# Performance work log

Measured on AMD Instinct MI355X. Metric: run time of the kernel, lower is better.

Reference implementation:

```python
import jax, jax.numpy as jnp
import numpy as np

EPS = float(np.finfo(np.float32).tiny)  # matches torch EPSILON
TAU = 0.1
K = 64  # self.k


def setup_inputs() -> dict:
    key = jax.random.key(0)
    k1, k2 = jax.random.split(key)
    bsz, Nmax, ensemble, train_ensemble = 64, 128, 2, 2
    scores = jax.random.normal(k1, (bsz, Nmax, Nmax, ensemble), dtype=jnp.float32)
    # Gumbel(0,1) noise, pre-sampled for determinism: g = -log(-log(U))
    u = jax.random.uniform(k2, (train_ensemble * bsz * ensemble, Nmax * Nmax),
                           dtype=jnp.float32, minval=1e-7, maxval=1.0 - 1e-7)
    gumbel = -jnp.log(-jnp.log(u))
    return {"scores": scores, "gumbel": gumbel, "train_ensemble": train_ensemble}


def reference(scores, gumbel, train_ensemble):
    # policy == 'global_topk_directed'
    bsz, Nmax, _, ensemble = scores.shape
    local_k = min(K, Nmax * Nmax)
    # (bsz, Nmax, Nmax, E) -> (bsz*E, Nmax^2)
    flat = scores.transpose(0, 3, 1, 2).reshape(bsz * ensemble, Nmax * Nmax)
    flat = jnp.tile(flat, (train_ensemble, 1)) + gumbel

    zeros = jnp.zeros_like(flat)

    def step(carry, _):
        f, khot, onehot = carry
        f = f + jnp.log(jnp.maximum(1.0 - onehot, EPS))
        onehot = jax.nn.softmax(f / TAU, axis=1)
        return (f, khot + onehot, onehot), None

    (flat, khot, _), _ = jax.lax.scan(step, (flat, zeros, zeros), None, length=local_k)

    # hard: straight-through k-hot via top-k scatter
    _, ind = jax.lax.top_k(khot, local_k)  # (R, local_k)
    rows = jnp.arange(khot.shape[0])[:, None]
    khot_hard = jnp.zeros_like(khot).at[rows, ind].set(1.0)
    res = khot_hard - jax.lax.stop_gradient(khot) + khot

    new_mask = res.reshape(train_ensemble, bsz, ensemble, Nmax, Nmax).transpose(0, 1, 3, 4, 2)
    return new_mask
```

## Files before the change

kernel.cpp:

```cpp
#include <hip/hip_runtime.h>
#include <math.h>


#define NWAVES  16
#define M_ELEMS 16384
#define EPT     16
#define KSEL    64
#define NCAND   256
#define CPL     4
#define NBINS   4096
#define THRESH  (M_ELEMS - NCAND)
#define C10     14.42695019f

template <int CTRL, int RM = 0xF>
__device__ __forceinline__ float dpp_f(float x, float identity) {
    return __int_as_float(__builtin_amdgcn_update_dpp(
        __float_as_int(identity), __float_as_int(x), CTRL, RM, 0xF, false));
}
template <int CTRL, int RM = 0xF>
__device__ __forceinline__ unsigned dpp_u(unsigned x, unsigned identity) {
    return (unsigned)__builtin_amdgcn_update_dpp(
        (int)identity, (int)x, CTRL, RM, 0xF, false);
}
__device__ __forceinline__ float wave_sum_bcast(float x) {
    x += dpp_f<0x111>(x, 0.0f);
    x += dpp_f<0x112>(x, 0.0f);
    x += dpp_f<0x114>(x, 0.0f);
    x += dpp_f<0x118>(x, 0.0f);
    x += dpp_f<0x142>(x, 0.0f);
    x += dpp_f<0x143>(x, 0.0f);
    return __int_as_float(__builtin_amdgcn_readlane(__float_as_int(x), 63));
}
__device__ __forceinline__ float wave_fmax_bcast(float x) {
    x = fmaxf(x, dpp_f<0x111>(x, -INFINITY));
    x = fmaxf(x, dpp_f<0x112>(x, -INFINITY));
    x = fmaxf(x, dpp_f<0x114>(x, -INFINITY));
    x = fmaxf(x, dpp_f<0x118>(x, -INFINITY));
    x = fmaxf(x, dpp_f<0x142>(x, -INFINITY));
    x = fmaxf(x, dpp_f<0x143>(x, -INFINITY));
    return __int_as_float(__builtin_amdgcn_readlane(__float_as_int(x), 63));
}
__device__ __forceinline__ unsigned wave_prefix_incl(unsigned x) {
    x += dpp_u<0x111>(x, 0u);
    x += dpp_u<0x112>(x, 0u);
    x += dpp_u<0x114>(x, 0u);
    x += dpp_u<0x118>(x, 0u);
    x += dpp_u<0x142, 0xA>(x, 0u);
    x += dpp_u<0x143, 0xC>(x, 0u);
    return x;
}

__global__ __launch_bounds__(1024, 4) void screen_kernel(
    const float* __restrict__ scores,
    const float* __restrict__ gumbel,
    float* __restrict__ cand_f,
    unsigned* __restrict__ cand_i,
    float* __restrict__ out)
{
    const int tid  = threadIdx.x;
    const int lane = tid & 63;
    const int wid  = tid >> 6;
    const int bid = blockIdx.x;
    const int r   = ((bid & 127) << 1) | (bid >> 7);
    const int t_ = r >> 7;
    const int be = r & 127;
    const int b  = be >> 1;
    const int e  = be & 1;

    __shared__ unsigned int hist[NBINS];
    __shared__ unsigned int wofs[NWAVES];
    __shared__ unsigned int cutbin;
    __shared__ unsigned int candcnt;

    float* orow = out + (size_t)(t_ * 64 + b) * (M_ELEMS * 2) + e;

    float fv[EPT];
    {
        const float* gum = gumbel + (size_t)r * M_ELEMS;
        const float* scb = scores + (size_t)b * (M_ELEMS * 2);
        #pragma unroll
        for (int g = 0; g < 4; ++g) {
            const int mb = (tid << 2) + (g << 12);
            const float4 gv = *reinterpret_cast<const float4*>(&gum[mb]);
            const float4 sa = *reinterpret_cast<const float4*>(&scb[(size_t)mb * 2]);
            const float4 sb = *reinterpret_cast<const float4*>(&scb[(size_t)mb * 2 + 4]);
            float s0, s1, s2, s3;
            if (e == 0) { s0 = sa.x; s1 = sa.z; s2 = sb.x; s3 = sb.z; }
            else        { s0 = sa.y; s1 = sa.w; s2 = sb.y; s3 = sb.w; }
            fv[g * 4 + 0] = s0 + gv.x;
            fv[g * 4 + 1] = s1 + gv.y;
            fv[g * 4 + 2] = s2 + gv.z;
            fv[g * 4 + 3] = s3 + gv.w;
        }
    }
    #pragma unroll
    for (int k = 0; k < NBINS / 1024; ++k) hist[tid + k * 1024] = 0u;
    __syncthreads();

    #pragma unroll
    for (int k = 0; k < EPT; ++k) {
        const unsigned u  = __float_as_uint(fv[k]);
        const unsigned tk = u ^ (unsigned)(((int)u >> 31) | 0x80000000);
        atomicAdd(&hist[tk >> 20], 1u);
    }
    __syncthreads();

    if (wid == 0) {
        unsigned part = 0;
        #pragma unroll 8
        for (int j = 0; j < 64; ++j)
            part += hist[(lane << 6) + ((j + lane) & 63)];
        const unsigned P = wave_prefix_incl(part);
        const unsigned long long mk = __ballot(P >= THRESH);
        const int L = __builtin_ctzll(mk);
        const unsigned base = (L > 0)
            ? (unsigned)__builtin_amdgcn_readlane((int)P, L - 1) : 0u;
        const unsigned h2 = hist[(L << 6) + lane];
        const unsigned p2 = wave_prefix_incl(h2) + base;
        const unsigned long long mk2 = __ballot(p2 >= THRESH);
        const int j2 = __builtin_ctzll(mk2);
        if (lane == 0) {
            cutbin  = (unsigned)((L << 6) + j2 + 1);
            candcnt = M_ELEMS - (unsigned)__builtin_amdgcn_readlane((int)p2, j2);
        }
    }
    __syncthreads();
    const unsigned cutKey = cutbin << 20;
    const unsigned nc     = candcnt;

    unsigned mycnt = 0, hitm = 0;
    #pragma unroll
    for (int k = 0; k < EPT; ++k) {
        const unsigned u  = __float_as_uint(fv[k]);
        const unsigned tk = u ^ (unsigned)(((int)u >> 31) | 0x80000000);
        const bool c = tk >= cutKey;
        hitm |= (c ? 1u : 0u) << k;
        mycnt += c ? 1u : 0u;
    }
    const unsigned inc = wave_prefix_incl(mycnt);
    if (lane == 63) wofs[wid] = inc;
    __syncthreads();
    unsigned wbase = 0;
    #pragma unroll
    for (int i = 0; i < NWAVES; ++i) wbase += (i < wid) ? wofs[i] : 0u;
    unsigned slot = wbase + inc - mycnt;
    float*    cfr = cand_f + (size_t)r * NCAND;
    unsigned* cir = cand_i + (size_t)r * NCAND;
    #pragma unroll
    for (int k = 0; k < EPT; ++k) {
        if ((hitm >> k) & 1u) {
            cfr[slot] = fv[k];
            cir[slot] = (unsigned)((tid << 2) + (k & 3) + ((k >> 2) << 12));
            ++slot;
        }
    }
    if ((unsigned)tid >= nc && tid < NCAND) {
        cfr[tid] = -INFINITY;
        cir[tid] = 0x7fffffffu;
    }

    #pragma unroll
    for (int k = 0; k < EPT; ++k)
        orow[(size_t)(tid + (k << 10)) * 2] = 0.0f;
}

__global__ __launch_bounds__(256, 8) void dyn_kernel(
    const float* __restrict__ cand_f,
    const unsigned* __restrict__ cand_i,
    float* __restrict__ out)
{
    const int tid  = threadIdx.x;
    const int lane = tid & 63;
    const int wid  = tid >> 6;
    const int r    = blockIdx.x;
    const int t_ = r >> 7;
    const int be = r & 127;
    const int b  = be >> 1;
    const int e  = be & 1;

    __shared__ __align__(16) float    khbuf[NCAND];
    __shared__ __align__(16) unsigned idxb[NCAND];

    float* orow = out + (size_t)(t_ * 64 + b) * (M_ELEMS * 2) + e;

    idxb[tid] = cand_i[(size_t)r * NCAND + tid];

    if (wid == 0) {
        float cf[CPL], cex[CPL], ckh[CPL];
        #pragma unroll
        for (int k = 0; k < CPL; ++k)
            cf[k] = cand_f[(size_t)r * NCAND + lane + (k << 6)];
        float cmax = fmaxf(fmaxf(cf[0], cf[1]), fmaxf(cf[2], cf[3]));
        cmax = wave_fmax_bcast(cmax);
        const float nbw = fmaf(-cmax, C10, 100.0f);
        #pragma unroll
        for (int k = 0; k < CPL; ++k) {
            cex[k] = __builtin_amdgcn_exp2f(fmaf(cf[k], C10, nbw));
            ckh[k] = 0.0f;
        }
        for (int it = 0; it < KSEL; ++it) {
            float gsum = wave_sum_bcast((cex[0] + cex[1]) + (cex[2] + cex[3]));
            const int eb = (int)((__float_as_uint(gsum) >> 23) & 0xFF);
            if (eb < 127 + 10) {
                int sh = 354 - eb;
                if (sh > 254) sh = 254;
                const float s = __uint_as_float((unsigned)sh << 23);
                #pragma unroll
                for (int k = 0; k < CPL; ++k) cex[k] *= s;
                gsum = wave_sum_bcast((cex[0] + cex[1]) + (cex[2] + cex[3]));
                if (!(gsum > 0.0f)) gsum = INFINITY;
            }
            const float rsum = __builtin_amdgcn_rcpf(gsum);
            #pragma unroll
            for (int k = 0; k < CPL; ++k) {
                ckh[k] = fmaf(cex[k], rsum, ckh[k]);
                const float t  = fmaf(-cex[k], rsum, 1.0f);
                const float t2 = t * t;
                const float t4 = t2 * t2;
                const float t8 = t4 * t4;
                cex[k] = cex[k] * t8 * t2;
            }
        }
        #pragma unroll
        for (int k = 0; k < CPL; ++k) khbuf[lane + (k << 6)] = ckh[k];
    }
    __syncthreads();

    const float    myv = khbuf[tid];
    const unsigned myi = idxb[tid];
    unsigned rank = 0;
    #pragma unroll 8
    for (int j = 0; j < NCAND; j += 4) {
        const float4 v  = *reinterpret_cast<const float4*>(&khbuf[j]);
        const uint4  ii = *reinterpret_cast<const uint4*>(&idxb[j]);
        rank += (v.x > myv || (v.x == myv && ii.x < myi)) ? 1u : 0u;
        rank += (v.y > myv || (v.y == myv && ii.y < myi)) ? 1u : 0u;
        rank += (v.z > myv || (v.z == myv && ii.z < myi)) ? 1u : 0u;
        rank += (v.w > myv || (v.w == myv && ii.w < myi)) ? 1u : 0u;
    }
    if (rank < KSEL && myi < M_ELEMS)
        orow[(size_t)myi * 2] = 1.0f;
}

extern "C" void kernel_launch(void* const* d_in, const int* in_sizes, int n_in,
                              void* d_out, int out_size, void* d_ws, size_t ws_size,
                              hipStream_t stream) {
    const float* scores = (const float*)d_in[0];
    const float* gumbel = (const float*)d_in[1];
    float* out = (float*)d_out;
    const int rows = in_sizes[1] / M_ELEMS;
    float*    cand_f = (float*)d_ws;
    unsigned* cand_i = (unsigned*)d_ws + (size_t)rows * NCAND;
    screen_kernel<<<rows, 1024, 0, stream>>>(scores, gumbel, cand_f, cand_i, out);
    dyn_kernel<<<rows, 256, 0, stream>>>(cand_f, cand_i, out);
}
```

Before: 36.54 us.

## Split screening of each row across two 512-thread blocks with per-half candidates

The screening kernel now runs two blocks per row, each handling half of the 16384 elements with 512 threads. Each half picks its own top 128 candidates through a histogram threshold, and these fill half of the 256-slot candidate buffer. The aim is more blocks for better occupancy and CU coverage (512 blocks instead of 256). In exchange, histogram zeroing and scanning work is duplicated, and correctness relies on the global top-64 lying within the union of the per-half top-128 sets, which always holds.

```diff
diff --git a/kernel.cpp b/kernel.cpp
--- a/kernel.cpp
+++ b/kernel.cpp
@@ -2,14 +2,15 @@
 #include <math.h>
 
 
-#define NWAVES  16
 #define M_ELEMS 16384
+#define HALF_N  8192
 #define EPT     16
 #define KSEL    64
+#define NCL     128
 #define NCAND   256
 #define CPL     4
 #define NBINS   4096
-#define THRESH  (M_ELEMS - NCAND)
+#define THRESH_L (HALF_N - NCL)
 #define C10     14.42695019f
 
 template <int CTRL, int RM = 0xF>
@@ -50,7 +51,7 @@
     return x;
 }
 
-__global__ __launch_bounds__(1024, 4) void screen_kernel(
+__global__ __launch_bounds__(512, 4) void screen_kernel(
     const float* __restrict__ scores,
     const float* __restrict__ gumbel,
     float* __restrict__ cand_f,
@@ -60,15 +61,17 @@
     const int tid  = threadIdx.x;
     const int lane = tid & 63;
     const int wid  = tid >> 6;
-    const int bid = blockIdx.x;
-    const int r   = ((bid & 127) << 1) | (bid >> 7);
+    const int bid  = blockIdx.x;
+    const int p    = bid & 255;
+    const int half = bid >> 8;
+    const int r    = ((p & 127) << 1) | (p >> 7);
     const int t_ = r >> 7;
     const int be = r & 127;
     const int b  = be >> 1;
     const int e  = be & 1;
 
     __shared__ unsigned int hist[NBINS];
-    __shared__ unsigned int wofs[NWAVES];
+    __shared__ unsigned int wofs[8];
     __shared__ unsigned int cutbin;
     __shared__ unsigned int candcnt;
 
@@ -80,7 +83,7 @@
         const float* scb = scores + (size_t)b * (M_ELEMS * 2);
         #pragma unroll
         for (int g = 0; g < 4; ++g) {
-            const int mb = (tid << 2) + (g << 12);
+            const int mb = (half << 13) + (tid << 2) + (g << 11);
             const float4 gv = *reinterpret_cast<const float4*>(&gum[mb]);
             const float4 sa = *reinterpret_cast<const float4*>(&scb[(size_t)mb * 2]);
             const float4 sb = *reinterpret_cast<const float4*>(&scb[(size_t)mb * 2 + 4]);
@@ -94,7 +97,7 @@
         }
     }
     #pragma unroll
-    for (int k = 0; k < NBINS / 1024; ++k) hist[tid + k * 1024] = 0u;
+    for (int k = 0; k < NBINS / 512; ++k) hist[tid + k * 512] = 0u;
     __syncthreads();
 
     #pragma unroll
@@ -111,17 +114,17 @@
         for (int j = 0; j < 64; ++j)
             part += hist[(lane << 6) + ((j + lane) & 63)];
         const unsigned P = wave_prefix_incl(part);
-        const unsigned long long mk = __ballot(P >= THRESH);
+        const unsigned long long mk = __ballot(P >= THRESH_L);
         const int L = __builtin_ctzll(mk);
         const unsigned base = (L > 0)
             ? (unsigned)__builtin_amdgcn_readlane((int)P, L - 1) : 0u;
         const unsigned h2 = hist[(L << 6) + lane];
         const unsigned p2 = wave_prefix_incl(h2) + base;
-        const unsigned long long mk2 = __ballot(p2 >= THRESH);
+        const unsigned long long mk2 = __ballot(p2 >= THRESH_L);
         const int j2 = __builtin_ctzll(mk2);
         if (lane == 0) {
             cutbin  = (unsigned)((L << 6) + j2 + 1);
-            candcnt = M_ELEMS - (unsigned)__builtin_amdgcn_readlane((int)p2, j2);
+            candcnt = HALF_N - (unsigned)__builtin_amdgcn_readlane((int)p2, j2);
         }
     }
     __syncthreads();
@@ -142,26 +145,28 @@
     __syncthreads();
     unsigned wbase = 0;
     #pragma unroll
-    for (int i = 0; i < NWAVES; ++i) wbase += (i < wid) ? wofs[i] : 0u;
+    for (int i = 0; i < 8; ++i) wbase += (i < wid) ? wofs[i] : 0u;
     unsigned slot = wbase + inc - mycnt;
-    float*    cfr = cand_f + (size_t)r * NCAND;
-    unsigned* cir = cand_i + (size_t)r * NCAND;
+    const size_t cbase = (size_t)r * NCAND + (size_t)half * NCL;
     #pragma unroll
     for (int k = 0; k < EPT; ++k) {
         if ((hitm >> k) & 1u) {
-            cfr[slot] = fv[k];
-            cir[slot] = (unsigned)((tid << 2) + (k & 3) + ((k >> 2) << 12));
+            cand_f[cbase + slot] = fv[k];
+            cand_i[cbase + slot] =
+                (unsigned)((half << 13) + (tid << 2) + (k & 3) + ((k >> 2) << 11));
             ++slot;
         }
     }
-    if ((unsigned)tid >= nc && tid < NCAND) {
-        cfr[tid] = -INFINITY;
-        cir[tid] = 0x7fffffffu;
-    }
-
-    #pragma unroll
-    for (int k = 0; k < EPT; ++k)
-        orow[(size_t)(tid + (k << 10)) * 2] = 0.0f;
+    if ((unsigned)tid >= nc && tid < NCL) {
+        cand_f[cbase + tid] = -INFINITY;
+        cand_i[cbase + tid] = 0x7fffffffu;
+    }
+
+    #pragma unroll
+    for (int k = 0; k < EPT; ++k) {
+        const int m = (half << 13) + tid + (k << 9);
+        orow[(size_t)m * 2] = 0.0f;
+    }
 }
 
 __global__ __launch_bounds__(256, 8) void dyn_kernel(
@@ -251,6 +256,6 @@
     const int rows = in_sizes[1] / M_ELEMS;
     float*    cand_f = (float*)d_ws;
     unsigned* cand_i = (unsigned*)d_ws + (size_t)rows * NCAND;
-    screen_kernel<<<rows, 1024, 0, stream>>>(scores, gumbel, cand_f, cand_i, out);
+    screen_kernel<<<rows * 2, 512, 0, stream>>>(scores, gumbel, cand_f, cand_i, out);
     dyn_kernel<<<rows, 256, 0, stream>>>(cand_f, cand_i, out);
 }
```

Measured after the change: 34.18 us. 1.07x faster.
